# Kernel tuning notes

Hardware: AMD Instinct MI355X
Metric: run time of the kernel (lower is better)

## Reference

```python
import jax, jax.numpy as jnp
import numpy as np

N, E, G = 20000, 320000, 8
H, C = 4, 64
NODE_IN, EDGE_IN, HID = 18, 4, 64
NEG = 0.2    # GATv2 leaky_relu negative slope
EPS = 1e-5   # BatchNorm eps (eval mode: running_mean=0, running_var=1)


def setup_inputs() -> dict:
    key = jax.random.key(0)
    ks = iter(jax.random.split(key, 48))
    rn = lambda shape, s=0.05: jax.random.normal(next(ks), shape, dtype=jnp.float32) * s
    return {
        "x": jax.random.normal(next(ks), (N, NODE_IN), dtype=jnp.float32),
        "edge_attr": jax.random.uniform(next(ks), (E, EDGE_IN), dtype=jnp.float32),
        "enc_w1": rn((NODE_IN, HID)), "enc_b1": jnp.zeros((HID,), jnp.float32),
        "enc_w2": rn((HID, HID)), "enc_b2": jnp.zeros((HID,), jnp.float32),
        "g1_wl": rn((HID, H * C)), "g1_wr": rn((HID, H * C)), "g1_we": rn((EDGE_IN, H * C)),
        "g1_att": rn((H, C)), "g1_b": jnp.zeros((H * C,), jnp.float32),
        "bn1_g": jnp.ones((H * C,), jnp.float32), "bn1_b": jnp.zeros((H * C,), jnp.float32),
        "g2_wl": rn((H * C, H * C)), "g2_wr": rn((H * C, H * C)), "g2_we": rn((EDGE_IN, H * C)),
        "g2_att": rn((H, C)), "g2_b": jnp.zeros((C,), jnp.float32),
        "bn2_g": jnp.ones((C,), jnp.float32), "bn2_b": jnp.zeros((C,), jnp.float32),
        "sage_wl": rn((HID, HID)), "sage_bl": jnp.zeros((HID,), jnp.float32), "sage_wr": rn((HID, HID)),
        "bn3_g": jnp.ones((HID,), jnp.float32), "bn3_b": jnp.zeros((HID,), jnp.float32),
        "gh_w1": rn((2 * HID, HID)), "gh_b1": jnp.zeros((HID,), jnp.float32),
        "gh_w2": rn((HID, 32)), "gh_b2": jnp.zeros((32,), jnp.float32),
        "gh_w3": rn((32, 1)), "gh_b3": jnp.zeros((1,), jnp.float32),
        "eh_w1": rn((2 * HID + EDGE_IN, 32)), "eh_b1": jnp.zeros((32,), jnp.float32),
        "eh_w2": rn((32, 1)), "eh_b2": jnp.zeros((1,), jnp.float32),
        "edge_index": jax.random.randint(next(ks), (2, E), 0, N, dtype=jnp.int32),
        "batch": jnp.sort(jax.random.randint(next(ks), (N,), 0, G, dtype=jnp.int32)),
    }


def _segment_softmax(logits, seg, num):
    mx = jax.ops.segment_max(logits, seg, num_segments=num)
    ex = jnp.exp(logits - mx[seg])
    den = jax.ops.segment_sum(ex, seg, num_segments=num)
    return ex / den[seg]


def _gatv2(h, src, dst, ea, wl, wr, we, att, bias, concat):
    n = h.shape[0]
    xl = (h @ wl).reshape(n, H, C)   # messages come from x_l[src]
    xr = (h @ wr).reshape(n, H, C)
    ee = (ea @ we).reshape(-1, H, C)
    m = xl[src] + xr[dst] + ee                                    # [E', H, C]
    logit = jnp.einsum('ehc,hc->eh', jax.nn.leaky_relu(m, NEG), att)
    alpha = _segment_softmax(logit, dst, n)                       # [E', H]
    out = jax.ops.segment_sum(alpha[:, :, None] * xl[src], dst, num_segments=n)
    if concat:
        return out.reshape(n, H * C) + bias
    return out.mean(axis=1) + bias


def _bn_eval(h, g, b):
    # eval-mode BatchNorm with running_mean=0, running_var=1
    return h * (g / jnp.sqrt(1.0 + EPS)) + b


def reference(x, edge_attr, enc_w1, enc_b1, enc_w2, enc_b2,
              g1_wl, g1_wr, g1_we, g1_att, g1_b, bn1_g, bn1_b,
              g2_wl, g2_wr, g2_we, g2_att, g2_b, bn2_g, bn2_b,
              sage_wl, sage_bl, sage_wr, bn3_g, bn3_b,
              gh_w1, gh_b1, gh_w2, gh_b2, gh_w3, gh_b3,
              eh_w1, eh_b1, eh_w2, eh_b2, edge_index, batch):
    src, dst = edge_index[0], edge_index[1]
    # PyG add_self_loops with fill_value='mean': loop edge_attr = mean of incoming edge_attr
    ones = jnp.ones((E,), jnp.float32)
    cnt = jax.ops.segment_sum(ones, dst, num_segments=N)
    loop_attr = jax.ops.segment_sum(edge_attr, dst, num_segments=N) / jnp.clip(cnt, 1.0)[:, None]
    sl = jnp.arange(N, dtype=src.dtype)
    src_sl = jnp.concatenate([src, sl])
    dst_sl = jnp.concatenate([dst, sl])
    ea_sl = jnp.concatenate([edge_attr, loop_attr], axis=0)

    # ZoneEncoder (dropout inactive in eval)
    h = jax.nn.relu(x @ enc_w1 + enc_b1) @ enc_w2 + enc_b2
    h = _gatv2(h, src_sl, dst_sl, ea_sl, g1_wl, g1_wr, g1_we, g1_att, g1_b, True)
    h = jax.nn.elu(_bn_eval(h, bn1_g, bn1_b))
    h = _gatv2(h, src_sl, dst_sl, ea_sl, g2_wl, g2_wr, g2_we, g2_att, g2_b, False)
    h = jax.nn.elu(_bn_eval(h, bn2_g, bn2_b))
    # SAGEConv: lin_l(mean_{j->i} h_j) + lin_r(h_i), no self loops
    agg = jax.ops.segment_sum(h[src], dst, num_segments=N) / jnp.clip(cnt, 1.0)[:, None]
    h = agg @ sage_wl + sage_bl + h @ sage_wr
    h = jax.nn.relu(_bn_eval(h, bn3_g, bn3_b))
    # global mean + max pooling per graph
    cntg = jax.ops.segment_sum(jnp.ones((N,), jnp.float32), batch, num_segments=G)
    mean_p = jax.ops.segment_sum(h, batch, num_segments=G) / jnp.clip(cntg, 1.0)[:, None]
    max_p = jax.ops.segment_max(h, batch, num_segments=G)
    hp = jnp.concatenate([mean_p, max_p], axis=-1)                # [G, 128]
    z = jax.nn.relu(hp @ gh_w1 + gh_b1)
    z = jax.nn.relu(z @ gh_w2 + gh_b2)
    graph_score = jax.nn.sigmoid(z @ gh_w3 + gh_b3)               # [G, 1]
    ef = jnp.concatenate([h[src], h[dst], edge_attr], axis=-1)    # [E, 132]
    ez = jax.nn.relu(ef @ eh_w1 + eh_b1)
    edge_scores = jax.nn.sigmoid(ez @ eh_w2 + eh_b2)              # [E, 1]
    return (graph_score, edge_scores)
```

## Files before the change

### kernel.cpp

```cpp
#include <hip/hip_runtime.h>

#define NN 20000
#define NE 320000
#define EP (NE + NN)
#define NG 8
#define HC 256
#define NODE_IN 18
#define HID 64
#define NEG_SLOPE 0.2f
#define BN_EPS 1e-5f

#define OFF_XL    0u
#define OFF_XR    5120000u
#define OFF_H1    10240000u
#define OFF_WTL   12800000u
#define OFF_WTR   12832768u
#define OFF_H3B   12865536u
#define OFF_WT1   13185536u
#define OFF_H0    15360000u
#define OFF_H3    16640000u
#define OFF_ZERO  18000000u
#define OFF_CNT   18000000u
#define OFF_PSUM  18020000u
#define OFF_PMAX  18020512u
#define OFF_PCNT  18021024u
#define ZERO_FLOATS (18021040u - 18000000u)
#define OFF_EACSR 18021040u
#define OFF_RP    19381040u
#define OFF_SRC   19421041u
#define OFF_BSUM  19761056u

#define SCAN_ELEM 1024
#define SCAN_NB ((NN + SCAN_ELEM - 1) / SCAN_ELEM)
#define NB32 (NN / 32)

#define PRE_CNT_NB 1250
#define PRE_CAST_NB 536
#define PRE_ENC_NB 1250
#define POST_EH_NB (NE / 64)
#define POST_POOL_NB ((NN + 255) / 256)

typedef __attribute__((ext_vector_type(8))) short bf16x8_t;
typedef __attribute__((ext_vector_type(4))) float f32x4_t;

__device__ __forceinline__ ushort f2bf(float f) {
  unsigned u = __float_as_uint(f);
  unsigned r = (u + 0x7fffu + ((u >> 16) & 1u)) >> 16;
  return (ushort)r;
}
__device__ __forceinline__ float bf2f(ushort b) {
  return __uint_as_float(((unsigned)b) << 16);
}

#define ENC_NPW 4
__global__ __launch_bounds__(256) void k_pre(
    const int* __restrict__ ei, unsigned* __restrict__ cnt, int* __restrict__ rank,
    const float* __restrict__ Wl, const float* __restrict__ Wr,
    const float* __restrict__ w1eh,
    ushort* __restrict__ WtL, ushort* __restrict__ WtR, ushort* __restrict__ wt1,
    const float* __restrict__ x, const float* __restrict__ ew1, const float* __restrict__ eb1,
    const float* __restrict__ ew2, const float* __restrict__ eb2, float* __restrict__ h0) {
  __shared__ float W1[NODE_IN * HID];
  __shared__ float W2[HID * HID];
  __shared__ float B1s[HID];
  __shared__ float B2s[HID];
  __shared__ float hid_s[4][HID];
  const int b = blockIdx.x;
  const int tid = threadIdx.x;
  if (b < PRE_CNT_NB) {
    int e = b * 256 + tid;
    if (e < NE) {
      int d = ei[NE + e];
      rank[e] = (int)atomicAdd(&cnt[d], 1u);
    }
    return;
  }
  if (b < PRE_CNT_NB + PRE_CAST_NB) {
    int bb = b - PRE_CNT_NB;
    if (bb < 512) {
      const float* W = (bb < 256) ? Wl : Wr;
      ushort* Wt = (bb < 256) ? WtL : WtR;
      int k = bb & 255;
      Wt[tid * 256 + k] = f2bf(W[k * 256 + tid]);
    } else {
      int idx = (bb - 512) * 256 + tid;
      int n = idx / 192, k = idx - n * 192;
      wt1[idx] = (k < 132) ? f2bf(w1eh[k * 32 + n]) : (ushort)0;
    }
    return;
  }
  const int eb = b - PRE_CNT_NB - PRE_CAST_NB;
  for (int i = tid; i < NODE_IN * HID; i += 256) W1[i] = ew1[i];
  for (int i = tid; i < HID * HID; i += 256) W2[i] = ew2[i];
  if (tid < HID) { B1s[tid] = eb1[tid]; B2s[tid] = eb2[tid]; }
  __syncthreads();
  const int lane = tid & 63;
  const int w = tid >> 6;
  #pragma unroll
  for (int t = 0; t < ENC_NPW; t++) {
    const int n = eb * (4 * ENC_NPW) + w * ENC_NPW + t;
    const float* xp = &x[(size_t)n * NODE_IN];
    float s = B1s[lane];
    #pragma unroll
    for (int i = 0; i < NODE_IN; i++) s += xp[i] * W1[i * HID + lane];
    hid_s[w][lane] = fmaxf(s, 0.f);
    float o = B2s[lane];
    #pragma unroll 8
    for (int k = 0; k < HID; k++) o += hid_s[w][k] * W2[k * HID + lane];
    h0[(size_t)n * HID + lane] = o;
  }
}

__global__ __launch_bounds__(256) void k_scan_blk(
    const unsigned* __restrict__ cnt, int* __restrict__ row_ptr, int* __restrict__ bsums) {
  __shared__ int wsum[4];
  const int tid = threadIdx.x, lane = tid & 63, w = tid >> 6;
  const int i0 = blockIdx.x * SCAN_ELEM + tid * 4;
  int v0 = (i0 + 0 < NN) ? ((int)cnt[i0 + 0] + 1) : 0;
  int v1 = (i0 + 1 < NN) ? ((int)cnt[i0 + 1] + 1) : 0;
  int v2 = (i0 + 2 < NN) ? ((int)cnt[i0 + 2] + 1) : 0;
  int v3 = (i0 + 3 < NN) ? ((int)cnt[i0 + 3] + 1) : 0;
  int tsum = v0 + v1 + v2 + v3;
  int incl = tsum;
  #pragma unroll
  for (int off = 1; off < 64; off <<= 1) {
    int t = __shfl_up(incl, off);
    if (lane >= off) incl += t;
  }
  if (lane == 63) wsum[w] = incl;
  __syncthreads();
  int p = incl - tsum;
  #pragma unroll
  for (int k = 0; k < 4; k++) if (k < w) p += wsum[k];
  if (i0 + 0 < NN) row_ptr[i0 + 0] = p;
  if (i0 + 1 < NN) row_ptr[i0 + 1] = p + v0;
  if (i0 + 2 < NN) row_ptr[i0 + 2] = p + v0 + v1;
  if (i0 + 3 < NN) row_ptr[i0 + 3] = p + v0 + v1 + v2;
  if (tid == 0) bsums[blockIdx.x] = wsum[0] + wsum[1] + wsum[2] + wsum[3];
}

__global__ __launch_bounds__(256) void k_scan_add(
    const int* __restrict__ bsums, int* __restrict__ row_ptr) {
  const int b = blockIdx.x, tid = threadIdx.x;
  int off = 0;
  for (int j = 0; j < b; j++) off += bsums[j];
  const int i0 = b * SCAN_ELEM + tid * 4;
  #pragma unroll
  for (int k = 0; k < 4; k++) {
    int i = i0 + k;
    if (i < NN) row_ptr[i] += off;
  }
  if (b == 0 && tid == 0) row_ptr[NN] = EP;
}

__global__ __launch_bounds__(256) void k_csr_scatter(
    const int* __restrict__ ei, const int* __restrict__ rank,
    const int* __restrict__ row_ptr, const float* __restrict__ ea,
    int* __restrict__ srcs, float* __restrict__ ea_csr) {
  int e = blockIdx.x * 256 + threadIdx.x;
  if (e >= NE) return;
  int s = ei[e], d = ei[NE + e];
  int p = row_ptr[d] + rank[e];
  srcs[p] = s;
  *(float4*)&ea_csr[(size_t)p * 4] = *(const float4*)&ea[(size_t)e * 4];
}

__global__ __launch_bounds__(256) void k_loop_row(
    const int* __restrict__ row_ptr, int* __restrict__ srcs, float* __restrict__ ea_csr) {
  int lane = threadIdx.x & 63, w = threadIdx.x >> 6;
  int i = blockIdx.x * 4 + w;
  int start = row_ptr[i], last = row_ptr[i + 1] - 1;
  float s = 0.f;
  int base = start * 4;
  int nfl = (last - start) * 4;
  for (int f = lane; f < nfl; f += 64) s += ea_csr[base + f];
  s += __shfl_xor(s, 4);
  s += __shfl_xor(s, 8);
  s += __shfl_xor(s, 16);
  s += __shfl_xor(s, 32);
  float c = (float)(last - start);
  if (c < 1.f) c = 1.f;
  if (lane < 4) ea_csr[(size_t)last * 4 + lane] = s / c;
  if (lane == 0) srcs[last] = i | (int)0x80000000;
}

__global__ __launch_bounds__(256) void k_gemm256_dual(
    const float* __restrict__ A, const float* __restrict__ Wl_, const float* __restrict__ Wr_,
    ushort* __restrict__ OUTbf, float* __restrict__ OUTf) {
  const bool first = blockIdx.x < NB32;
  const float* __restrict__ W = first ? Wl_ : Wr_;
  const int n0 = (first ? blockIdx.x : blockIdx.x - NB32) * 32;
  __shared__ float Wlds[32 * 256];
  __shared__ float Al[32 * 36];
  const int tid = threadIdx.x;
  const int tx = tid & 63, ty = tid >> 6;
  float acc[8][4];
  #pragma unroll
  for (int m = 0; m < 8; m++)
    #pragma unroll
    for (int c = 0; c < 4; c++) acc[m][c] = 0.f;

  for (int kt = 0; kt < 64; kt += 32) {
    #pragma unroll
    for (int r = 0; r < 8; r++) {
      int i4 = tid + 256 * r;
      int row = i4 >> 6;
      int col4 = (i4 & 63) * 4;
      *(float4*)&Wlds[row * 256 + col4] = *(const float4*)&W[(size_t)(kt + row) * 256 + col4];
    }
    {
      int m = tid >> 3, kk = (tid & 7) * 4;
      float4 av = *(const float4*)&A[(size_t)(n0 + m) * 64 + kt + kk];
      Al[(kk + 0) * 36 + m] = av.x;
      Al[(kk + 1) * 36 + m] = av.y;
      Al[(kk + 2) * 36 + m] = av.z;
      Al[(kk + 3) * 36 + m] = av.w;
    }
    __syncthreads();
    #pragma unroll 8
    for (int k = 0; k < 32; k++) {
      float4 b = *(float4*)&Wlds[k * 256 + tx * 4];
      float4 a0v = *(float4*)&Al[k * 36 + ty * 8];
      float4 a1v = *(float4*)&Al[k * 36 + ty * 8 + 4];
      float am[8] = {a0v.x, a0v.y, a0v.z, a0v.w, a1v.x, a1v.y, a1v.z, a1v.w};
      #pragma unroll
      for (int m = 0; m < 8; m++) {
        acc[m][0] += am[m] * b.x;
        acc[m][1] += am[m] * b.y;
        acc[m][2] += am[m] * b.z;
        acc[m][3] += am[m] * b.w;
      }
    }
    __syncthreads();
  }
  if (first) {
    #pragma unroll
    for (int m = 0; m < 8; m++) {
      ushort4 o = {f2bf(acc[m][0]), f2bf(acc[m][1]), f2bf(acc[m][2]), f2bf(acc[m][3])};
      *(ushort4*)&OUTbf[(size_t)(n0 + ty * 8 + m) * 256 + tx * 4] = o;
    }
  } else {
    #pragma unroll
    for (int m = 0; m < 8; m++) {
      float4 o = {acc[m][0], acc[m][1], acc[m][2], acc[m][3]};
      *(float4*)&OUTf[(size_t)(n0 + ty * 8 + m) * 256 + tx * 4] = o;
    }
  }
}

__global__ __launch_bounds__(256) void k_gemm_mfma_dual(
    const ushort* __restrict__ A, const ushort* __restrict__ wtl,
    const ushort* __restrict__ wtr, ushort* __restrict__ OUTbf, float* __restrict__ OUTf) {
  const bool first = blockIdx.x < NB32;
  const ushort* __restrict__ Wt = first ? wtl : wtr;
  const int n0 = (first ? blockIdx.x : blockIdx.x - NB32) * 32;
  __shared__ ushort Asub[32][72];
  __shared__ ushort Wsub[256][72];
  const int tid = threadIdx.x;
  const int lane = tid & 63;
  const int w = tid >> 6;
  const int lr = lane & 15;
  const int lk = (lane >> 4) * 8;

  f32x4_t acc[2][4];
  #pragma unroll
  for (int m = 0; m < 2; m++)
    #pragma unroll
    for (int n = 0; n < 4; n++) acc[m][n] = (f32x4_t){0.f, 0.f, 0.f, 0.f};

  for (int kt = 0; kt < 256; kt += 64) {
    {
      int r = tid >> 3, seg = (tid & 7) * 8;
      *(uint4*)&Asub[r][seg] = *(const uint4*)&A[(size_t)(n0 + r) * 256 + kt + seg];
    }
    #pragma unroll
    for (int rep = 0; rep < 8; rep++) {
      int idx = rep * 256 + tid;
      int r = idx >> 3, seg = (idx & 7) * 8;
      *(uint4*)&Wsub[r][seg] = *(const uint4*)&Wt[(size_t)r * 256 + kt + seg];
    }
    __syncthreads();
    #pragma unroll
    for (int kk = 0; kk < 2; kk++) {
      bf16x8_t af0 = *(bf16x8_t*)&Asub[lr][kk * 32 + lk];
      bf16x8_t af1 = *(bf16x8_t*)&Asub[16 + lr][kk * 32 + lk];
      #pragma unroll
      for (int n = 0; n < 4; n++) {
        bf16x8_t bfr = *(bf16x8_t*)&Wsub[w * 64 + n * 16 + lr][kk * 32 + lk];
        acc[0][n] = __builtin_amdgcn_mfma_f32_16x16x32_bf16(af0, bfr, acc[0][n], 0, 0, 0);
        acc[1][n] = __builtin_amdgcn_mfma_f32_16x16x32_bf16(af1, bfr, acc[1][n], 0, 0, 0);
      }
    }
    __syncthreads();
  }
  const int crow = (lane >> 4) * 4;
  #pragma unroll
  for (int m = 0; m < 2; m++) {
    #pragma unroll
    for (int n = 0; n < 4; n++) {
      int col = w * 64 + n * 16 + lr;
      #pragma unroll
      for (int r = 0; r < 4; r++) {
        int row = n0 + m * 16 + crow + r;
        if (first) OUTbf[(size_t)row * 256 + col] = f2bf(acc[m][n][r]);
        else       OUTf[(size_t)row * 256 + col] = acc[m][n][r];
      }
    }
  }
}

#define GAT_EDGE(A_, U_, DN_, C0_, C1_, C2_, C3_)                                  \
  {                                                                                \
    float xx_ = bf2f((U_).x), xy_ = bf2f((U_).y), xz_ = bf2f((U_).z), xw_ = bf2f((U_).w); \
    float m0_ = xx_ + xrd.x + (A_).x * we0.x + (A_).y * we1.x + (A_).z * we2.x + (A_).w * we3.x; \
    float m1_ = xy_ + xrd.y + (A_).x * we0.y + (A_).y * we1.y + (A_).z * we2.y + (A_).w * we3.y; \
    float m2_ = xz_ + xrd.z + (A_).x * we0.z + (A_).y * we1.z + (A_).z * we2.z + (A_).w * we3.z; \
    float m3_ = xw_ + xrd.w + (A_).x * we0.w + (A_).y * we1.w + (A_).z * we2.w + (A_).w * we3.w; \
    m0_ = fmaxf(m0_, NEG_SLOPE * m0_);                                             \
    m1_ = fmaxf(m1_, NEG_SLOPE * m1_);                                             \
    m2_ = fmaxf(m2_, NEG_SLOPE * m2_);                                             \
    m3_ = fmaxf(m3_, NEG_SLOPE * m3_);                                             \
    float lg_ = m0_ * attv.x + m1_ * attv.y + m2_ * attv.z + m3_ * attv.w;         \
    lg_ += __shfl_xor(lg_, 1);                                                     \
    lg_ += __shfl_xor(lg_, 2);                                                     \
    lg_ += __shfl_xor(lg_, 4);                                                     \
    lg_ += __shfl_xor(lg_, 8);                                                     \
    float p_ = __expf(lg_);                                                        \
    DN_ += p_;                                                                     \
    C0_ = fmaf(p_, xx_, C0_);                                                      \
    C1_ = fmaf(p_, xy_, C1_);                                                      \
    C2_ = fmaf(p_, xz_, C2_);                                                      \
    C3_ = fmaf(p_, xw_, C3_);                                                      \
  }

template <int CONCAT>
__global__ __launch_bounds__(256) void k_gat_fused(
    const ushort* __restrict__ xl, const float* __restrict__ xr,
    const float* __restrict__ we, const float* __restrict__ att,
    const int* __restrict__ srcs, const float* __restrict__ ea_csr,
    const int* __restrict__ row_ptr,
    const float* __restrict__ bias, const float* __restrict__ bng,
    const float* __restrict__ bnb, void* __restrict__ outp) {
  const int lane = threadIdx.x & 63;
  const int w = threadIdx.x >> 6;
  const int i = blockIdx.x * 4 + w;
  const int c0 = lane * 4;

  const float4 attv = *(const float4*)&att[c0];
  const float4 we0 = *(const float4*)&we[0 * HC + c0];
  const float4 we1 = *(const float4*)&we[1 * HC + c0];
  const float4 we2 = *(const float4*)&we[2 * HC + c0];
  const float4 we3 = *(const float4*)&we[3 * HC + c0];
  const float4 xrd = *(const float4*)&xr[(size_t)i * HC + c0];

  const int start = row_ptr[i];
  const int deg = row_ptr[i + 1] - start;

  float dnA = 0.f, aA0 = 0.f, aA1 = 0.f, aA2 = 0.f, aA3 = 0.f;
  float dnB = 0.f, aB0 = 0.f, aB1 = 0.f, aB2 = 0.f, aB3 = 0.f;

  for (int base = 0; base < deg; base += 64) {
    int rem = deg - base;
    if (rem > 64) rem = 64;
    int sv = 0;
    if (lane < rem) sv = srcs[start + base + lane] & 0x7fffffff;
    int jj = 0;
    for (; jj + 2 <= rem; jj += 2) {
      int s0 = __shfl(sv, jj);
      int s1 = __shfl(sv, jj + 1);
      float4 a0 = *(const float4*)&ea_csr[(size_t)(start + base + jj) * 4];
      float4 a1 = *(const float4*)&ea_csr[(size_t)(start + base + jj + 1) * 4];
      ushort4 u0 = *(const ushort4*)&xl[(size_t)s0 * HC + c0];
      ushort4 u1 = *(const ushort4*)&xl[(size_t)s1 * HC + c0];
      GAT_EDGE(a0, u0, dnA, aA0, aA1, aA2, aA3);
      GAT_EDGE(a1, u1, dnB, aB0, aB1, aB2, aB3);
    }
    if (jj < rem) {
      int s0 = __shfl(sv, jj);
      float4 a0 = *(const float4*)&ea_csr[(size_t)(start + base + jj) * 4];
      ushort4 u0 = *(const ushort4*)&xl[(size_t)s0 * HC + c0];
      GAT_EDGE(a0, u0, dnA, aA0, aA1, aA2, aA3);
    }
  }

  float rinv = 1.f / (dnA + dnB);
  float acc0 = (aA0 + aB0) * rinv;
  float acc1 = (aA1 + aB1) * rinv;
  float acc2 = (aA2 + aB2) * rinv;
  float acc3 = (aA3 + aB3) * rinv;

  const float inv_sqrt = rsqrtf(1.f + BN_EPS);
  if (CONCAT) {
    float4 bi = *(const float4*)&bias[c0];
    float4 g = *(const float4*)&bng[c0];
    float4 bb = *(const float4*)&bnb[c0];
    float v0 = (acc0 + bi.x) * (g.x * inv_sqrt) + bb.x;
    float v1 = (acc1 + bi.y) * (g.y * inv_sqrt) + bb.y;
    float v2 = (acc2 + bi.z) * (g.z * inv_sqrt) + bb.z;
    float v3 = (acc3 + bi.w) * (g.w * inv_sqrt) + bb.w;
    v0 = (v0 > 0.f) ? v0 : (__expf(v0) - 1.f);
    v1 = (v1 > 0.f) ? v1 : (__expf(v1) - 1.f);
    v2 = (v2 > 0.f) ? v2 : (__expf(v2) - 1.f);
    v3 = (v3 > 0.f) ? v3 : (__expf(v3) - 1.f);
    ushort* op = (ushort*)outp;
    ushort4 o = {f2bf(v0), f2bf(v1), f2bf(v2), f2bf(v3)};
    *(ushort4*)&op[(size_t)i * HC + c0] = o;
  } else {
    acc0 += __shfl_xor(acc0, 16); acc0 += __shfl_xor(acc0, 32);
    acc1 += __shfl_xor(acc1, 16); acc1 += __shfl_xor(acc1, 32);
    acc2 += __shfl_xor(acc2, 16); acc2 += __shfl_xor(acc2, 32);
    acc3 += __shfl_xor(acc3, 16); acc3 += __shfl_xor(acc3, 32);
    if (lane < 16) {
      int cc = lane * 4;
      float4 bi = *(const float4*)&bias[cc];
      float4 g = *(const float4*)&bng[cc];
      float4 bb = *(const float4*)&bnb[cc];
      float v0 = (0.25f * acc0 + bi.x) * (g.x * inv_sqrt) + bb.x;
      float v1 = (0.25f * acc1 + bi.y) * (g.y * inv_sqrt) + bb.y;
      float v2 = (0.25f * acc2 + bi.z) * (g.z * inv_sqrt) + bb.z;
      float v3 = (0.25f * acc3 + bi.w) * (g.w * inv_sqrt) + bb.w;
      v0 = (v0 > 0.f) ? v0 : (__expf(v0) - 1.f);
      v1 = (v1 > 0.f) ? v1 : (__expf(v1) - 1.f);
      v2 = (v2 > 0.f) ? v2 : (__expf(v2) - 1.f);
      v3 = (v3 > 0.f) ? v3 : (__expf(v3) - 1.f);
      float* op = (float*)outp;
      float4 o = {v0, v1, v2, v3};
      *(float4*)&op[(size_t)i * 64 + cc] = o;
    }
  }
}

__global__ __launch_bounds__(256) void k_sage(
    const float* __restrict__ h2, const int* __restrict__ row_ptr,
    const int* __restrict__ srcs, const unsigned* __restrict__ cnt,
    const float* __restrict__ wl, const float* __restrict__ bl,
    const float* __restrict__ wr, const float* __restrict__ bng,
    const float* __restrict__ bnb, float* __restrict__ h3,
    ushort* __restrict__ h3b) {
  __shared__ float agg_s[4][64];
  __shared__ float h2_s[4][64];
  int lane = threadIdx.x & 63;
  int w = threadIdx.x >> 6;
  int i = blockIdx.x * 4 + w;
  int start = row_ptr[i];
  int nreal = row_ptr[i + 1] - 1 - start;
  float a0 = 0.f, a1 = 0.f, a2 = 0.f, a3 = 0.f;
  for (int base = 0; base < nreal; base += 64) {
    int rem = nreal - base;
    if (rem > 64) rem = 64;
    int sv = 0;
    if (lane < rem) sv = srcs[start + base + lane];
    int jj = 0;
    for (; jj + 4 <= rem; jj += 4) {
      int s0 = __shfl(sv, jj);
      int s1 = __shfl(sv, jj + 1);
      int s2 = __shfl(sv, jj + 2);
      int s3 = __shfl(sv, jj + 3);
      a0 += h2[(size_t)s0 * 64 + lane];
      a1 += h2[(size_t)s1 * 64 + lane];
      a2 += h2[(size_t)s2 * 64 + lane];
      a3 += h2[(size_t)s3 * 64 + lane];
    }
    for (; jj < rem; ++jj) {
      int s0 = __shfl(sv, jj);
      a0 += h2[(size_t)s0 * 64 + lane];
    }
  }
  float a = (a0 + a1) + (a2 + a3);
  float c = (float)cnt[i];
  if (c < 1.f) c = 1.f;
  agg_s[w][lane] = a / c;
  h2_s[w][lane] = h2[(size_t)i * 64 + lane];
  __syncthreads();
  float s = bl[lane];
  #pragma unroll 4
  for (int k = 0; k < 64; k++)
    s += agg_s[w][k] * wl[k * 64 + lane] + h2_s[w][k] * wr[k * 64 + lane];
  s = s * (bng[lane] * rsqrtf(1.f + BN_EPS)) + bnb[lane];
  s = fmaxf(s, 0.f);
  h3[(size_t)i * 64 + lane] = s;
  h3b[(size_t)i * 64 + lane] = f2bf(s);
}

__global__ __launch_bounds__(256) void k_post(
    const ushort* __restrict__ h3b, const int* __restrict__ ei,
    const float* __restrict__ ea, const ushort* __restrict__ wt1,
    const float* __restrict__ b1, const float* __restrict__ w2,
    const float* __restrict__ b2, float* __restrict__ out,
    const float* __restrict__ h3, const int* __restrict__ batch,
    float* __restrict__ psum, float* __restrict__ pmax, float* __restrict__ pcnt) {
  const int tid = threadIdx.x;
  if (blockIdx.x >= POST_EH_NB) {
    int pb = blockIdx.x - POST_EH_NB;
    int j = tid & 63, grp = tid >> 6;
    int nbase = pb * 256 + grp * 64;
    float s = 0.f, m = 0.f, cn = 0.f;
    int cur = -1;
    for (int t = 0; t < 64; t++) {
      int n = nbase + t;
      if (n >= NN) break;
      int g = batch[n];
      if (g != cur) {
        if (cur >= 0) {
          atomicAdd(&psum[cur * 64 + j], s);
          atomicMax((int*)&pmax[cur * 64 + j], __float_as_int(m));
          if (j == 0) atomicAdd(&pcnt[cur], cn);
        }
        cur = g; s = 0.f; m = 0.f; cn = 0.f;
      }
      float v = h3[(size_t)n * 64 + j];
      s += v; m = fmaxf(m, v); cn += 1.f;
    }
    if (cur >= 0) {
      atomicAdd(&psum[cur * 64 + j], s);
      atomicMax((int*)&pmax[cur * 64 + j], __float_as_int(m));
      if (j == 0) atomicAdd(&pcnt[cur], cn);
    }
    return;
  }
  const int lane = tid & 63, wid = tid >> 6;
  const int lr = lane & 15, hi = lane >> 4, lk = hi * 8;
  const int e = blockIdx.x * 64 + wid * 16 + lr;
  const int sn = ei[e], dn = ei[NE + e];
  const ushort* hs = &h3b[(size_t)sn * 64];
  const ushort* hd = &h3b[(size_t)dn * 64];
  bf16x8_t a0f = *(const bf16x8_t*)&hs[lk];
  bf16x8_t a1f = *(const bf16x8_t*)&hs[32 + lk];
  bf16x8_t a2f = *(const bf16x8_t*)&hd[lk];
  bf16x8_t a3f = *(const bf16x8_t*)&hd[32 + lk];
  bf16x8_t a4f = (bf16x8_t){0, 0, 0, 0, 0, 0, 0, 0};
  if (hi == 0) {
    float4 a = *(const float4*)&ea[(size_t)e * 4];
    a4f[0] = (short)f2bf(a.x);
    a4f[1] = (short)f2bf(a.y);
    a4f[2] = (short)f2bf(a.z);
    a4f[3] = (short)f2bf(a.w);
  }
  f32x4_t acc0 = (f32x4_t){0.f, 0.f, 0.f, 0.f};
  f32x4_t acc1 = (f32x4_t){0.f, 0.f, 0.f, 0.f};
  #pragma unroll
  for (int ks = 0; ks < 5; ks++) {
    bf16x8_t af = (ks == 0) ? a0f : (ks == 1) ? a1f : (ks == 2) ? a2f : (ks == 3) ? a3f : a4f;
    bf16x8_t bw0 = *(const bf16x8_t*)&wt1[(size_t)lr * 192 + ks * 32 + lk];
    bf16x8_t bw1 = *(const bf16x8_t*)&wt1[(size_t)(16 + lr) * 192 + ks * 32 + lk];
    acc0 = __builtin_amdgcn_mfma_f32_16x16x32_bf16(af, bw0, acc0, 0, 0, 0);
    acc1 = __builtin_amdgcn_mfma_f32_16x16x32_bf16(af, bw1, acc1, 0, 0, 0);
  }
  float b1c0 = b1[lr], b1c1 = b1[16 + lr];
  float w2c0 = w2[lr], w2c1 = w2[16 + lr];
  float part[4];
  #pragma unroll
  for (int r = 0; r < 4; r++) {
    float v0 = fmaxf(acc0[r] + b1c0, 0.f) * w2c0;
    float v1 = fmaxf(acc1[r] + b1c1, 0.f) * w2c1;
    float p = v0 + v1;
    p += __shfl_xor(p, 1);
    p += __shfl_xor(p, 2);
    p += __shfl_xor(p, 4);
    p += __shfl_xor(p, 8);
    part[r] = p;
  }
  if (lr == 0) {
    const float bb2 = b2[0];
    int ebase = blockIdx.x * 64 + wid * 16 + hi * 4;
    #pragma unroll
    for (int r = 0; r < 4; r++)
      out[ebase + r] = 1.f / (1.f + __expf(-(part[r] + bb2)));
  }
}

__global__ void k_graph_head(
    const float* __restrict__ psum, const float* __restrict__ pmax,
    const float* __restrict__ pcnt,
    const float* __restrict__ w1, const float* __restrict__ b1,
    const float* __restrict__ w2, const float* __restrict__ b2,
    const float* __restrict__ w3, const float* __restrict__ b3,
    float* __restrict__ out) {
  __shared__ float hp[128];
  __shared__ float z1[64];
  __shared__ float z2[32];
  int g = blockIdx.x, j = threadIdx.x;
  float c = pcnt[g];
  if (c < 1.f) c = 1.f;
  hp[j] = psum[g * 64 + j] / c;
  hp[64 + j] = pmax[g * 64 + j];
  __syncthreads();
  float s = b1[j];
  #pragma unroll 8
  for (int k = 0; k < 128; k++) s += hp[k] * w1[k * 64 + j];
  z1[j] = fmaxf(s, 0.f);
  __syncthreads();
  if (j < 32) {
    float s2 = b2[j];
    #pragma unroll 8
    for (int k = 0; k < 64; k++) s2 += z1[k] * w2[k * 32 + j];
    z2[j] = fmaxf(s2, 0.f);
  }
  __syncthreads();
  if (j == 0) {
    float s3 = b3[0];
    #pragma unroll
    for (int k = 0; k < 32; k++) s3 += z2[k] * w3[k];
    out[g] = 1.f / (1.f + expf(-s3));
  }
}

extern "C" void kernel_launch(void* const* d_in, const int* in_sizes, int n_in,
                              void* d_out, int out_size, void* d_ws, size_t ws_size,
                              hipStream_t stream) {
  const float* x         = (const float*)d_in[0];
  const float* edge_attr = (const float*)d_in[1];
  const float* enc_w1 = (const float*)d_in[2];
  const float* enc_b1 = (const float*)d_in[3];
  const float* enc_w2 = (const float*)d_in[4];
  const float* enc_b2 = (const float*)d_in[5];
  const float* g1_wl = (const float*)d_in[6];
  const float* g1_wr = (const float*)d_in[7];
  const float* g1_we = (const float*)d_in[8];
  const float* g1_att = (const float*)d_in[9];
  const float* g1_b = (const float*)d_in[10];
  const float* bn1_g = (const float*)d_in[11];
  const float* bn1_b = (const float*)d_in[12];
  const float* g2_wl = (const float*)d_in[13];
  const float* g2_wr = (const float*)d_in[14];
  const float* g2_we = (const float*)d_in[15];
  const float* g2_att = (const float*)d_in[16];
  const float* g2_b = (const float*)d_in[17];
  const float* bn2_g = (const float*)d_in[18];
  const float* bn2_b = (const float*)d_in[19];
  const float* sage_wl = (const float*)d_in[20];
  const float* sage_bl = (const float*)d_in[21];
  const float* sage_wr = (const float*)d_in[22];
  const float* bn3_g = (const float*)d_in[23];
  const float* bn3_b = (const float*)d_in[24];
  const float* gh_w1 = (const float*)d_in[25];
  const float* gh_b1 = (const float*)d_in[26];
  const float* gh_w2 = (const float*)d_in[27];
  const float* gh_b2 = (const float*)d_in[28];
  const float* gh_w3 = (const float*)d_in[29];
  const float* gh_b3 = (const float*)d_in[30];
  const float* eh_w1 = (const float*)d_in[31];
  const float* eh_b1 = (const float*)d_in[32];
  const float* eh_w2 = (const float*)d_in[33];
  const float* eh_b2 = (const float*)d_in[34];
  const int* ei    = (const int*)d_in[35];
  const int* batch = (const int*)d_in[36];
  float* out = (float*)d_out;

  float* ws = (float*)d_ws;
  ushort* xlbf = (ushort*)(ws + OFF_XL);
  float* xr = ws + OFF_XR;
  ushort* h1bf = (ushort*)(ws + OFF_H1);
  ushort* wtl = (ushort*)(ws + OFF_WTL);
  ushort* wtr = (ushort*)(ws + OFF_WTR);
  ushort* h3b = (ushort*)(ws + OFF_H3B);
  ushort* wt1e = (ushort*)(ws + OFF_WT1);
  float* h0 = ws + OFF_H0;
  float* h3 = ws + OFF_H3;
  unsigned* cnt = (unsigned*)(ws + OFF_CNT);
  float* psum = ws + OFF_PSUM;
  float* pmax = ws + OFF_PMAX;
  float* pcnt = ws + OFF_PCNT;
  float* ea_csr = ws + OFF_EACSR;
  int* row_ptr = (int*)(ws + OFF_RP);
  int* srcs = (int*)(ws + OFF_SRC);
  int* bsums = (int*)(ws + OFF_BSUM);
  int* rank = (int*)(ws + OFF_XL);

  hipMemsetAsync(ws + OFF_ZERO, 0, ZERO_FLOATS * sizeof(float), stream);

  k_pre<<<PRE_CNT_NB + PRE_CAST_NB + PRE_ENC_NB, 256, 0, stream>>>(
      ei, cnt, rank, g2_wl, g2_wr, eh_w1, wtl, wtr, wt1e,
      x, enc_w1, enc_b1, enc_w2, enc_b2, h0);
  k_scan_blk<<<SCAN_NB, 256, 0, stream>>>(cnt, row_ptr, bsums);
  k_scan_add<<<SCAN_NB, 256, 0, stream>>>(bsums, row_ptr);
  k_csr_scatter<<<NE / 256, 256, 0, stream>>>(ei, rank, row_ptr, edge_attr, srcs, ea_csr);
  k_loop_row<<<NN / 4, 256, 0, stream>>>(row_ptr, srcs, ea_csr);

  k_gemm256_dual<<<2 * NB32, 256, 0, stream>>>(h0, g1_wl, g1_wr, xlbf, xr);
  k_gat_fused<1><<<NN / 4, 256, 0, stream>>>(xlbf, xr, g1_we, g1_att, srcs, ea_csr,
                                             row_ptr, g1_b, bn1_g, bn1_b, (void*)h1bf);

  k_gemm_mfma_dual<<<2 * NB32, 256, 0, stream>>>(h1bf, wtl, wtr, xlbf, xr);
  k_gat_fused<0><<<NN / 4, 256, 0, stream>>>(xlbf, xr, g2_we, g2_att, srcs, ea_csr,
                                             row_ptr, g2_b, bn2_g, bn2_b, (void*)h0);

  k_sage<<<NN / 4, 256, 0, stream>>>(h0, row_ptr, srcs, cnt, sage_wl, sage_bl, sage_wr,
                                     bn3_g, bn3_b, h3, h3b);

  k_post<<<POST_EH_NB + POST_POOL_NB, 256, 0, stream>>>(
      h3b, ei, edge_attr, wt1e, eh_b1, eh_w2, eh_b2, out + NG,
      h3, batch, psum, pmax, pcnt);
  k_graph_head<<<NG, 64, 0, stream>>>(psum, pmax, pcnt, gh_w1, gh_b1, gh_w2, gh_b2, gh_w3, gh_b3, out);
}
```

Measured before the change: 323.7 us.

## Precompute per-node edge-head projections in SAGE kernel, gather them per edge

The edge head's first layer is split algebraically: h[src]@W1[0:64] and h[dst]@W1[64:128] are computed once per node inside k_sage and stored as a 64-wide fp32 projection table. k_post then only gathers two 32-float slices per edge, adds the edge_attr contribution and bias, and applies ReLU, the second layer and the sigmoid in scalar code, one edge per thread. This replaces the per-edge bf16 MFMA over 132 inputs and drops the bf16 weight cast and the h3 bf16 copy. In exchange, the per-edge gathers are fp32 (256 bytes per edge instead of 256 bytes of bf16 h3), and each k_sage block now loads a 16KB weight tile into LDS.

Measured after the change: 311.7 us. 1.04x faster.

```diff
diff --git a/kernel.cpp b/kernel.cpp
--- a/kernel.cpp
+++ b/kernel.cpp
@@ -15,8 +15,7 @@
 #define OFF_H1    10240000u
 #define OFF_WTL   12800000u
 #define OFF_WTR   12832768u
-#define OFF_H3B   12865536u
-#define OFF_WT1   13185536u
+#define OFF_P     13200000u
 #define OFF_H0    15360000u
 #define OFF_H3    16640000u
 #define OFF_ZERO  18000000u
@@ -35,9 +34,9 @@
 #define NB32 (NN / 32)
 
 #define PRE_CNT_NB 1250
-#define PRE_CAST_NB 536
+#define PRE_CAST_NB 512
 #define PRE_ENC_NB 1250
-#define POST_EH_NB (NE / 64)
+#define POST_EH_NB (NE / 256)
 #define POST_POOL_NB ((NN + 255) / 256)
 
 typedef __attribute__((ext_vector_type(8))) short bf16x8_t;
@@ -56,8 +55,7 @@
 __global__ __launch_bounds__(256) void k_pre(
     const int* __restrict__ ei, unsigned* __restrict__ cnt, int* __restrict__ rank,
     const float* __restrict__ Wl, const float* __restrict__ Wr,
-    const float* __restrict__ w1eh,
-    ushort* __restrict__ WtL, ushort* __restrict__ WtR, ushort* __restrict__ wt1,
+    ushort* __restrict__ WtL, ushort* __restrict__ WtR,
     const float* __restrict__ x, const float* __restrict__ ew1, const float* __restrict__ eb1,
     const float* __restrict__ ew2, const float* __restrict__ eb2, float* __restrict__ h0) {
   __shared__ float W1[NODE_IN * HID];
@@ -77,16 +75,10 @@
   }
   if (b < PRE_CNT_NB + PRE_CAST_NB) {
     int bb = b - PRE_CNT_NB;
-    if (bb < 512) {
-      const float* W = (bb < 256) ? Wl : Wr;
-      ushort* Wt = (bb < 256) ? WtL : WtR;
-      int k = bb & 255;
-      Wt[tid * 256 + k] = f2bf(W[k * 256 + tid]);
-    } else {
-      int idx = (bb - 512) * 256 + tid;
-      int n = idx / 192, k = idx - n * 192;
-      wt1[idx] = (k < 132) ? f2bf(w1eh[k * 32 + n]) : (ushort)0;
-    }
+    const float* W = (bb < 256) ? Wl : Wr;
+    ushort* Wt = (bb < 256) ? WtL : WtR;
+    int k = bb & 255;
+    Wt[tid * 256 + k] = f2bf(W[k * 256 + tid]);
     return;
   }
   const int eb = b - PRE_CNT_NB - PRE_CAST_NB;
@@ -435,12 +427,18 @@
     const int* __restrict__ srcs, const unsigned* __restrict__ cnt,
     const float* __restrict__ wl, const float* __restrict__ bl,
     const float* __restrict__ wr, const float* __restrict__ bng,
-    const float* __restrict__ bnb, float* __restrict__ h3,
-    ushort* __restrict__ h3b) {
+    const float* __restrict__ bnb, const float* __restrict__ w1eh,
+    float* __restrict__ h3, float* __restrict__ P) {
+  __shared__ float Wc[64][64];
   __shared__ float agg_s[4][64];
   __shared__ float h2_s[4][64];
-  int lane = threadIdx.x & 63;
-  int w = threadIdx.x >> 6;
+  int tid = threadIdx.x;
+  for (int idx = tid; idx < 4096; idx += 256) {
+    int k = idx >> 6, j = idx & 63;
+    Wc[k][j] = (j < 32) ? w1eh[k * 32 + j] : w1eh[(64 + k) * 32 + (j - 32)];
+  }
+  int lane = tid & 63;
+  int w = tid >> 6;
   int i = blockIdx.x * 4 + w;
   int start = row_ptr[i];
   int nreal = row_ptr[i + 1] - 1 - start;
@@ -479,12 +477,16 @@
   s = s * (bng[lane] * rsqrtf(1.f + BN_EPS)) + bnb[lane];
   s = fmaxf(s, 0.f);
   h3[(size_t)i * 64 + lane] = s;
-  h3b[(size_t)i * 64 + lane] = f2bf(s);
+  agg_s[w][lane] = s;
+  float p = 0.f;
+  #pragma unroll 4
+  for (int k = 0; k < 64; k++) p += agg_s[w][k] * Wc[k][lane];
+  P[(size_t)i * 64 + lane] = p;
 }
 
 __global__ __launch_bounds__(256) void k_post(
-    const ushort* __restrict__ h3b, const int* __restrict__ ei,
-    const float* __restrict__ ea, const ushort* __restrict__ wt1,
+    const float* __restrict__ P, const int* __restrict__ ei,
+    const float* __restrict__ ea, const float* __restrict__ w1eh,
     const float* __restrict__ b1, const float* __restrict__ w2,
     const float* __restrict__ b2, float* __restrict__ out,
     const float* __restrict__ h3, const int* __restrict__ batch,
@@ -518,55 +520,31 @@
     }
     return;
   }
-  const int lane = tid & 63, wid = tid >> 6;
-  const int lr = lane & 15, hi = lane >> 4, lk = hi * 8;
-  const int e = blockIdx.x * 64 + wid * 16 + lr;
+  const int e = blockIdx.x * 256 + tid;
   const int sn = ei[e], dn = ei[NE + e];
-  const ushort* hs = &h3b[(size_t)sn * 64];
-  const ushort* hd = &h3b[(size_t)dn * 64];
-  bf16x8_t a0f = *(const bf16x8_t*)&hs[lk];
-  bf16x8_t a1f = *(const bf16x8_t*)&hs[32 + lk];
-  bf16x8_t a2f = *(const bf16x8_t*)&hd[lk];
-  bf16x8_t a3f = *(const bf16x8_t*)&hd[32 + lk];
-  bf16x8_t a4f = (bf16x8_t){0, 0, 0, 0, 0, 0, 0, 0};
-  if (hi == 0) {
-    float4 a = *(const float4*)&ea[(size_t)e * 4];
-    a4f[0] = (short)f2bf(a.x);
-    a4f[1] = (short)f2bf(a.y);
-    a4f[2] = (short)f2bf(a.z);
-    a4f[3] = (short)f2bf(a.w);
-  }
-  f32x4_t acc0 = (f32x4_t){0.f, 0.f, 0.f, 0.f};
-  f32x4_t acc1 = (f32x4_t){0.f, 0.f, 0.f, 0.f};
-  #pragma unroll
-  for (int ks = 0; ks < 5; ks++) {
-    bf16x8_t af = (ks == 0) ? a0f : (ks == 1) ? a1f : (ks == 2) ? a2f : (ks == 3) ? a3f : a4f;
-    bf16x8_t bw0 = *(const bf16x8_t*)&wt1[(size_t)lr * 192 + ks * 32 + lk];
-    bf16x8_t bw1 = *(const bf16x8_t*)&wt1[(size_t)(16 + lr) * 192 + ks * 32 + lk];
-    acc0 = __builtin_amdgcn_mfma_f32_16x16x32_bf16(af, bw0, acc0, 0, 0, 0);
-    acc1 = __builtin_amdgcn_mfma_f32_16x16x32_bf16(af, bw1, acc1, 0, 0, 0);
-  }
-  float b1c0 = b1[lr], b1c1 = b1[16 + lr];
-  float w2c0 = w2[lr], w2c1 = w2[16 + lr];
-  float part[4];
-  #pragma unroll
-  for (int r = 0; r < 4; r++) {
-    float v0 = fmaxf(acc0[r] + b1c0, 0.f) * w2c0;
-    float v1 = fmaxf(acc1[r] + b1c1, 0.f) * w2c1;
-    float p = v0 + v1;
-    p += __shfl_xor(p, 1);
-    p += __shfl_xor(p, 2);
-    p += __shfl_xor(p, 4);
-    p += __shfl_xor(p, 8);
-    part[r] = p;
-  }
-  if (lr == 0) {
-    const float bb2 = b2[0];
-    int ebase = blockIdx.x * 64 + wid * 16 + hi * 4;
-    #pragma unroll
-    for (int r = 0; r < 4; r++)
-      out[ebase + r] = 1.f / (1.f + __expf(-(part[r] + bb2)));
-  }
+  const float* Ps = &P[(size_t)sn * 64];
+  const float* Pd = &P[(size_t)dn * 64 + 32];
+  float acc[32];
+  #pragma unroll
+  for (int f = 0; f < 8; f++) {
+    float4 p1 = *(const float4*)&Ps[f * 4];
+    float4 p2 = *(const float4*)&Pd[f * 4];
+    acc[f * 4 + 0] = p1.x + p2.x;
+    acc[f * 4 + 1] = p1.y + p2.y;
+    acc[f * 4 + 2] = p1.z + p2.z;
+    acc[f * 4 + 3] = p1.w + p2.w;
+  }
+  float4 av = *(const float4*)&ea[(size_t)e * 4];
+  const float* w1c = &w1eh[128 * 32];
+  float z = 0.f;
+  #pragma unroll
+  for (int j = 0; j < 32; j++) {
+    float v = acc[j] + b1[j]
+            + av.x * w1c[j] + av.y * w1c[32 + j]
+            + av.z * w1c[64 + j] + av.w * w1c[96 + j];
+    z += fmaxf(v, 0.f) * w2[j];
+  }
+  out[e] = 1.f / (1.f + __expf(-(z + b2[0])));
 }
 
 __global__ void k_graph_head(
@@ -653,8 +631,7 @@
   ushort* h1bf = (ushort*)(ws + OFF_H1);
   ushort* wtl = (ushort*)(ws + OFF_WTL);
   ushort* wtr = (ushort*)(ws + OFF_WTR);
-  ushort* h3b = (ushort*)(ws + OFF_H3B);
-  ushort* wt1e = (ushort*)(ws + OFF_WT1);
+  float* Pproj = ws + OFF_P;
   float* h0 = ws + OFF_H0;
   float* h3 = ws + OFF_H3;
   unsigned* cnt = (unsigned*)(ws + OFF_CNT);
@@ -670,7 +647,7 @@
   hipMemsetAsync(ws + OFF_ZERO, 0, ZERO_FLOATS * sizeof(float), stream);
 
   k_pre<<<PRE_CNT_NB + PRE_CAST_NB + PRE_ENC_NB, 256, 0, stream>>>(
-      ei, cnt, rank, g2_wl, g2_wr, eh_w1, wtl, wtr, wt1e,
+      ei, cnt, rank, g2_wl, g2_wr, wtl, wtr,
       x, enc_w1, enc_b1, enc_w2, enc_b2, h0);
   k_scan_blk<<<SCAN_NB, 256, 0, stream>>>(cnt, row_ptr, bsums);
   k_scan_add<<<SCAN_NB, 256, 0, stream>>>(bsums, row_ptr);
@@ -686,10 +663,10 @@
                                              row_ptr, g2_b, bn2_g, bn2_b, (void*)h0);
 
   k_sage<<<NN / 4, 256, 0, stream>>>(h0, row_ptr, srcs, cnt, sage_wl, sage_bl, sage_wr,
-                                     bn3_g, bn3_b, h3, h3b);
+                                     bn3_g, bn3_b, eh_w1, h3, Pproj);
 
   k_post<<<POST_EH_NB + POST_POOL_NB, 256, 0, stream>>>(
-      h3b, ei, edge_attr, wt1e, eh_b1, eh_w2, eh_b2, out + NG,
+      Pproj, ei, edge_attr, eh_w1, eh_b1, eh_w2, eh_b2, out + NG,
       h3, batch, psum, pmax, pcnt);
   k_graph_head<<<NG, 64, 0, stream>>>(psum, pmax, pcnt, gh_w1, gh_b1, gh_w2, gh_b2, gh_w3, gh_b3, out);
 }
```
